# Optimization experiments

Measured on AMD Instinct MI355X. Metric: run time of the kernel, lower is better.

Reference implementation:

```python
import jax, jax.numpy as jnp
import numpy as np

B_DIM, C_DIM, K_DIM, L_DIM = 16, 64, 207, 64
SUPPORT_LEN, ORDER = 2, 2
C_IN = (ORDER * SUPPORT_LEN + 1) * C_DIM  # 320, include_self=True


def setup_inputs() -> dict:
    key = jax.random.key(0)
    k1, k2, k3, k4 = jax.random.split(key, 4)
    x = jax.random.normal(k1, (B_DIM, C_DIM, K_DIM * L_DIM), dtype=jnp.float32)
    # per-batch adaptive adjacencies (B, K, K), nonnegative like softmax(relu(E1 E2^T))
    a0 = jax.random.uniform(k2, (B_DIM, K_DIM, K_DIM), dtype=jnp.float32)
    a1 = jax.random.uniform(k3, (B_DIM, K_DIM, K_DIM), dtype=jnp.float32)
    # 1x1 conv weight (C_out, C_in) and bias
    W = jax.random.normal(k4, (C_DIM, C_IN), dtype=jnp.float32) * (1.0 / np.sqrt(C_IN))
    b = jnp.zeros((C_DIM,), dtype=jnp.float32)
    return {"x": x, "a0": a0, "a1": a1, "W": W, "b": b, "K": K_DIM, "L": L_DIM}


def reference(x, a0, a1, W, b, K, L):
    B, C = x.shape[0], x.shape[1]
    x = x.reshape(B, C, K, L)  # (B, C, K, L)
    # torch: x1[bl, c, j] = sum_k x[bl, c, k] * a[b, j, k]  (bmm with a^T)
    diffuse = lambda h, a: jnp.einsum('bckl,bjk->bcjl', h, a)
    out = [x]  # include_self=True
    for a in (a0, a1):
        x1 = diffuse(x, a)
        out.append(x1)
        for _ in range(2, ORDER + 1):
            x1 = diffuse(x1, a)
            out.append(x1)
    h = jnp.concatenate(out, axis=1)  # (B, 5C, K, L)
    y = jnp.einsum('bikl,oi->bokl', h, W) + b[None, :, None, None]  # 1x1 conv
    return y.reshape(B, C, K * L)
```

## Files before the change

### kernel.cpp

```cpp
#include <hip/hip_runtime.h>

typedef unsigned short u16;
typedef __bf16 bf16x8 __attribute__((ext_vector_type(8)));
typedef float f32x4 __attribute__((ext_vector_type(4)));

#define NB 16
#define NC 64
#define NK 207
#define NL 64
#define KP 224
#define NKL 13248
#define CIN 320


__device__ __forceinline__ u16 f2bf(float f) {
  unsigned u = __builtin_bit_cast(unsigned, f);
  u += 0x7FFFu + ((u >> 16) & 1u);
  return (u16)(u >> 16);
}

__device__ __forceinline__ void g2l16(const u16* gsrc, u16* ldst) {
  __builtin_amdgcn_global_load_lds(
      (const __attribute__((address_space(1))) unsigned int*)gsrc,
      (__attribute__((address_space(3))) unsigned int*)ldst, 16, 0, 0);
}

__global__ __launch_bounds__(256) void k_prep(
    const float* __restrict__ x, const float* __restrict__ a0,
    const float* __restrict__ a1, const float* __restrict__ W,
    u16* __restrict__ Xf, u16* __restrict__ Gf, u16* __restrict__ Wbf) {
  __shared__ __align__(16) u16 sm[32768];
  int id = blockIdx.x, t = threadIdx.x;
  if (id < 448) {
    int ks = id % 7;
    int rest = id / 7;
    int c4b = rest & 3, b = rest >> 2;
    int cl = t & 15, kp = t >> 4;
    int c = c4b * 16 + cl;
    int k0 = ks * 32 + kp * 2;
    const float* xrow = x + (size_t)(b * 64 + c) * NKL + (size_t)k0 * 64;
    bool in0 = (k0 < NK), in1 = (k0 + 1 < NK);
    unsigned* sm32 = (unsigned*)sm;
    int fi = (cl + 16 * (kp >> 2)) * 4 + (kp & 3);
#pragma unroll
    for (int g = 0; g < 4; g++) {
      float4 v0[4], v1[4];
#pragma unroll
      for (int i = 0; i < 4; i++) {
        float4 z = {0.f, 0.f, 0.f, 0.f};
        v0[i] = in0 ? *(const float4*)(xrow + g * 16 + i * 4) : z;
        v1[i] = in1 ? *(const float4*)(xrow + 64 + g * 16 + i * 4) : z;
      }
      const float* f0 = (const float*)v0;
      const float* f1 = (const float*)v1;
#pragma unroll
      for (int e2 = 0; e2 < 16; e2++) {
        int ll = g * 16 + e2;
        sm32[ll * 256 + fi] =
            (unsigned)f2bf(f0[e2]) | ((unsigned)f2bf(f1[e2]) << 16);
      }
    }
    __syncthreads();
    int wavei = t >> 6, lane = t & 63;
    u16* Xb = Xf + (size_t)b * 256 * 7 * 512;
    for (int f = wavei * 16; f < wavei * 16 + 16; f++) {
      bf16x8 v = *(const bf16x8*)&sm[f * 512 + lane * 8];
      *(bf16x8*)(Xb + ((size_t)(f * 4 + c4b) * 7 + ks) * 512 + lane * 8) = v;
    }
  } else if (id < 960) {
    int local = id - 448;
    int bw = local >> 4, tp = local & 15;
    int b = bw >> 1, w = bw & 1;
    int m0 = (tp >> 2) * 64, n0 = (tp & 3) * 64;
    const float* A = (w ? a1 : a0) + (size_t)b * NK * NK;
    for (int u = t; u < 64 * 28; u += 256) {
      int ml = u / 28, kc = u - ml * 28;
      int m = m0 + ml;
      u16 v[8] __attribute__((aligned(16)));
#pragma unroll
      for (int j = 0; j < 8; j++) {
        int k = kc * 8 + j;
        v[j] = (m < NK && k < NK) ? f2bf(A[(size_t)m * NK + k]) : (u16)0;
      }
      *(int4*)&sm[((ml >> 4) * 7 + (kc >> 2)) * 512 +
                  ((ml & 15) + 16 * (kc & 3)) * 8] = *(int4*)v;
    }
    {
      int nl = t & 63, mq = t >> 6;
      int n = n0 + nl;
      bool nin = (n < NK);
      unsigned* cm32 = (unsigned*)&sm[14336];
      for (int mi = 0; mi < 28; mi++) {
        int m = mq * 56 + mi * 2;
        u16 lo = (nin && m < NK) ? f2bf(A[(size_t)m * NK + n]) : (u16)0;
        u16 hi = (nin && m + 1 < NK) ? f2bf(A[(size_t)(m + 1) * NK + n]) : (u16)0;
        cm32[((nl >> 4) * 7 + (m >> 5)) * 256 +
             ((nl & 15) + 16 * ((m >> 3) & 3)) * 4 + ((m >> 1) & 3)] =
            (unsigned)lo | ((unsigned)hi << 16);
      }
    }
    __syncthreads();
    int lane = t & 63, wave = t >> 6;
    int r = lane & 15, q = lane >> 4;
    u16* Gp24 = Gf + ((size_t)b * 5 + 2 + 2 * w) * 13 * 7 * 512;
    for (int o = wave; o < 16; o += 4) {
      int mf = o >> 2, nf = o & 3;
      f32x4 acc = {};
#pragma unroll
      for (int ks = 0; ks < 7; ks++) {
        bf16x8 af = *(const bf16x8*)&sm[(mf * 7 + ks) * 512 + lane * 8];
        bf16x8 bg = *(const bf16x8*)&sm[14336 + (nf * 7 + ks) * 512 + lane * 8];
        acc = __builtin_amdgcn_mfma_f32_16x16x32_bf16(af, bg, acc, 0, 0, 0);
      }
#pragma unroll
      for (int rr = 0; rr < 4; rr++) {
        int mj = m0 + mf * 16 + q * 4 + rr;
        int nk = n0 + nf * 16 + r;
        if (mj < 208 && nk < KP)
          Gp24[((size_t)(mj >> 4) * 7 + (nk >> 5)) * 512 +
               ((mj & 15) + 16 * ((nk >> 3) & 3)) * 8 + (nk & 7)] =
              f2bf(acc[rr]);
      }
    }
  } else if (id < 1216) {
    int local = id - 960;
    int rt = local & 7, bw = local >> 3;
    int b = bw >> 1, w = bw & 1;
    const float* A = (w ? a1 : a0) + (size_t)b * NK * NK;
    u16* Gp13 = Gf + ((size_t)b * 5 + 1 + 2 * w) * 13 * 7 * 512;
    int m0 = rt * 26;
    for (int u = t; u < 26 * 28; u += 256) {
      int ml = u / 28, kc = u - ml * 28;
      int m = m0 + ml;
      u16 v[8] __attribute__((aligned(16)));
#pragma unroll
      for (int j = 0; j < 8; j++) {
        int k = kc * 8 + j;
        v[j] = (m < NK && k < NK) ? f2bf(A[(size_t)m * NK + k]) : (u16)0;
      }
      *(int4*)(Gp13 + ((size_t)(m >> 4) * 7 + (kc >> 2)) * 512 +
               ((m & 15) + 16 * (kc & 3)) * 8) = *(int4*)v;
    }
  } else if (id < 1248) {
    int local = id - 1216, b = local >> 1, half = local & 1;
    u16* Gp0 = Gf + (size_t)b * 5 * 13 * 7 * 512;
    for (int ci = t; ci < 104 * 28; ci += 256) {
      int jr = ci / 28, kc = ci - jr * 28;
      int j = half * 104 + jr;
      u16 v[8] __attribute__((aligned(16)));
      for (int jj = 0; jj < 8; jj++)
        v[jj] = (j == kc * 8 + jj && j < NK) ? (u16)0x3F80 : (u16)0;
      *(int4*)(Gp0 + ((size_t)(j >> 4) * 7 + (kc >> 2)) * 512 +
               ((j & 15) + 16 * (kc & 3)) * 8) = *(int4*)v;
    }
  } else {
    for (int ci = t; ci < 2560; ci += 256) {
      int o = ci / 40, kc = ci - o * 40;
      u16 v[8] __attribute__((aligned(16)));
      for (int j = 0; j < 8; j++) v[j] = f2bf(W[o * CIN + kc * 8 + j]);
      *(int4*)(Wbf + ((size_t)(o >> 4) * 10 + (kc >> 2)) * 512 +
               ((o & 15) + 16 * (kc & 3)) * 8) = *(int4*)v;
    }
  }
}

#define AG 17920
__global__ __launch_bounds__(512, 4) void k_fused(
    const u16* __restrict__ Gf, const u16* __restrict__ Xf,
    const u16* __restrict__ Wbf, const float* __restrict__ bias,
    float* __restrict__ y) {
  __shared__ __align__(16) u16 lds[AG + 2 * 8192];
  int id = blockIdx.x;
  int wg = (id & 7) * 416 + (id >> 3);
  int b = wg / 208, rem = wg % 208;
  int jt = rem >> 4, lt = rem & 15;
  int tid = threadIdx.x, wave = tid >> 6, lane = tid & 63;
  int r = lane & 15, q = lane >> 4;
  const u16* Gb = Gf + (size_t)b * 5 * 13 * 7 * 512;
  const u16* Xw = Xf + ((size_t)b * 256 + lt * 16) * 7 * 512;

  for (int i2 = 0; i2 < 5; i2++) {
    int tile = i2 * 8 + wave;
    if (tile < 35) {
      int p = tile / 7, ks = tile - p * 7;
      g2l16(Gb + ((size_t)(p * 13 + jt) * 7 + ks) * 512 + lane * 8,
            &lds[tile * 512 + lane * 8]);
    }
  }
  for (int i2 = 0; i2 < 2; i2++) {
    int tl = wave * 2 + i2;
    g2l16(Xw + (size_t)tl * 7 * 512 + lane * 8, &lds[AG + tl * 512 + lane * 8]);
  }
  asm volatile("s_waitcnt vmcnt(2)" ::: "memory");
  __builtin_amdgcn_s_barrier();

  f32x4 acc1[5][2] = {};
#pragma unroll
  for (int ks = 0; ks < 7; ks++) {
    int cur = ks & 1;
    if (ks < 6) {
      for (int i2 = 0; i2 < 2; i2++) {
        int tl = wave * 2 + i2;
        g2l16(Xw + ((size_t)tl * 7 + ks + 1) * 512 + lane * 8,
              &lds[AG + (cur ^ 1) * 8192 + tl * 512 + lane * 8]);
      }
      asm volatile("s_waitcnt vmcnt(2)" ::: "memory");
    } else {
      asm volatile("s_waitcnt vmcnt(0)" ::: "memory");
    }
    bf16x8 af0 = *(const bf16x8*)&lds[AG + cur * 8192 + (wave * 2 + 0) * 512 + lane * 8];
    bf16x8 af1 = *(const bf16x8*)&lds[AG + cur * 8192 + (wave * 2 + 1) * 512 + lane * 8];
    __builtin_amdgcn_s_setprio(1);
#pragma unroll
    for (int p = 0; p < 5; p++) {
      bf16x8 bg = *(const bf16x8*)&lds[(p * 7 + ks) * 512 + lane * 8];
      acc1[p][0] = __builtin_amdgcn_mfma_f32_16x16x32_bf16(af0, bg, acc1[p][0], 0, 0, 0);
      acc1[p][1] = __builtin_amdgcn_mfma_f32_16x16x32_bf16(af1, bg, acc1[p][1], 0, 0, 0);
    }
    __builtin_amdgcn_s_setprio(0);
  }
  __syncthreads();

#pragma unroll
  for (int p = 0; p < 5; p++)
#pragma unroll
    for (int mf = 0; mf < 2; mf++) {
      int m = (wave * 2 + mf) * 16 + q * 4;
      int tt = m >> 6, c = m & 63;
      int cs = c ^ ((r & 7) << 3);
      int idxT = ((p * 16 + r) * 4 + tt) * 72 + cs;
      u16 v0 = f2bf(acc1[p][mf][0]), v1 = f2bf(acc1[p][mf][1]);
      u16 v2 = f2bf(acc1[p][mf][2]), v3 = f2bf(acc1[p][mf][3]);
      *(uint2*)&lds[idxT] = make_uint2((unsigned)v0 | ((unsigned)v1 << 16),
                                       (unsigned)v2 | ((unsigned)v3 << 16));
    }
  int mo = wave >> 1, nh = (wave & 1) * 2;
  const u16* Wt = Wbf + (size_t)mo * 10 * 512 + lane * 8;
  bf16x8 aw[10];
#pragma unroll
  for (int ks = 0; ks < 10; ks++) aw[ks] = *(const bf16x8*)(Wt + ks * 512);
  __syncthreads();

  f32x4 acc2[2] = {};
#pragma unroll
  for (int ks = 0; ks < 10; ks++) {
    int p = ks >> 1, c0 = (ks & 1) * 32;
#pragma unroll
    for (int nf = 0; nf < 2; nf++) {
      int n = (nh + nf) * 16 + r;
      int j = n >> 2, tt = n & 3;
      int cs = (c0 + q * 8) ^ ((j & 7) << 3);
      bf16x8 bt = *(const bf16x8*)&lds[((p * 16 + j) * 4 + tt) * 72 + cs];
      acc2[nf] = __builtin_amdgcn_mfma_f32_16x16x32_bf16(aw[ks], bt, acc2[nf], 0, 0, 0);
    }
  }

  int o0 = mo * 16 + q * 4;
  float4 bv = *(const float4*)&bias[o0];
  float* yb = y + (size_t)b * 64 * NKL;
#pragma unroll
  for (int nf = 0; nf < 2; nf++) {
    int n = (nh + nf) * 16 + r;
    int j = n >> 2, tt = n & 3;
    int jnode = jt * 16 + j;
    if (jnode < NK) {
      int col = jnode * 64 + lt * 4 + tt;
      yb[(size_t)(o0 + 0) * NKL + col] = acc2[nf][0] + bv.x;
      yb[(size_t)(o0 + 1) * NKL + col] = acc2[nf][1] + bv.y;
      yb[(size_t)(o0 + 2) * NKL + col] = acc2[nf][2] + bv.z;
      yb[(size_t)(o0 + 3) * NKL + col] = acc2[nf][3] + bv.w;
    }
  }
}

extern "C" void kernel_launch(void* const* d_in, const int* in_sizes, int n_in,
                              void* d_out, int out_size, void* d_ws, size_t ws_size,
                              hipStream_t stream) {
  const float* x = (const float*)d_in[0];
  const float* a0 = (const float*)d_in[1];
  const float* a1 = (const float*)d_in[2];
  const float* W = (const float*)d_in[3];
  const float* bias = (const float*)d_in[4];
  float* y = (float*)d_out;
  char* ws = (char*)d_ws;

  size_t off = 0;
  auto alloc = [&](size_t bytes) {
    size_t o = off;
    off = (off + bytes + 511) & ~(size_t)511;
    return o;
  };
  size_t o_Xf = alloc((size_t)NB * 256 * 7 * 512 * 2);
  size_t o_Gf = alloc((size_t)NB * 5 * 13 * 7 * 512 * 2);
  size_t o_Wf = alloc((size_t)4 * 10 * 512 * 2);
  (void)ws_size;

  u16* Xf = (u16*)(ws + o_Xf);
  u16* Gf = (u16*)(ws + o_Gf);
  u16* Wf = (u16*)(ws + o_Wf);

  k_prep<<<dim3(1249), 256, 0, stream>>>(x, a0, a1, W, Xf, Gf, Wf);
  k_fused<<<dim3(16 * 13 * 16), 512, 0, stream>>>(Gf, Xf, Wf, bias, y);
}
```

Measured before the change: 235.9 us.

## Split prep kernel into finer blocks with smaller shared memory footprint

```diff
diff --git a/kernel.cpp b/kernel.cpp
--- a/kernel.cpp
+++ b/kernel.cpp
@@ -29,51 +29,52 @@
     const float* __restrict__ x, const float* __restrict__ a0,
     const float* __restrict__ a1, const float* __restrict__ W,
     u16* __restrict__ Xf, u16* __restrict__ Gf, u16* __restrict__ Wbf) {
-  __shared__ __align__(16) u16 sm[32768];
+  __shared__ __align__(16) u16 sm[14336];
   int id = blockIdx.x, t = threadIdx.x;
-  if (id < 448) {
+  if (id < 1792) {
     int ks = id % 7;
     int rest = id / 7;
-    int c4b = rest & 3, b = rest >> 2;
-    int cl = t & 15, kp = t >> 4;
-    int c = c4b * 16 + cl;
-    int k0 = ks * 32 + kp * 2;
-    const float* xrow = x + (size_t)(b * 64 + c) * NKL + (size_t)k0 * 64;
-    bool in0 = (k0 < NK), in1 = (k0 + 1 < NK);
-    unsigned* sm32 = (unsigned*)sm;
-    int fi = (cl + 16 * (kp >> 2)) * 4 + (kp & 3);
-#pragma unroll
-    for (int g = 0; g < 4; g++) {
-      float4 v0[4], v1[4];
-#pragma unroll
-      for (int i = 0; i < 4; i++) {
-        float4 z = {0.f, 0.f, 0.f, 0.f};
-        v0[i] = in0 ? *(const float4*)(xrow + g * 16 + i * 4) : z;
-        v1[i] = in1 ? *(const float4*)(xrow + 64 + g * 16 + i * 4) : z;
-      }
-      const float* f0 = (const float*)v0;
-      const float* f1 = (const float*)v1;
-#pragma unroll
-      for (int e2 = 0; e2 < 16; e2++) {
-        int ll = g * 16 + e2;
-        sm32[ll * 256 + fi] =
-            (unsigned)f2bf(f0[e2]) | ((unsigned)f2bf(f1[e2]) << 16);
-      }
+    int lh = rest & 3, c4 = (rest >> 2) & 3, b = rest >> 4;
+    int l0 = lh * 16;
+    int cl = t & 15, kl = t >> 4;
+    const float* xc = x + (size_t)(b * 64 + c4 * 16 + cl) * NKL;
+#pragma unroll
+    for (int kki = 0; kki < 2; kki++) {
+      int kk = kl + kki * 16;
+      int k = ks * 32 + kk;
+      float4 v0 = {0.f, 0.f, 0.f, 0.f}, v1 = v0, v2 = v0, v3 = v0;
+      if (k < NK) {
+        const float4* p = (const float4*)(xc + (size_t)k * 64 + l0);
+        v0 = p[0]; v1 = p[1]; v2 = p[2]; v3 = p[3];
+      }
+      int q = kk >> 3, e = kk & 7;
+      u16* dst = &sm[(cl + 16 * q) * 8 + e];
+      dst[0 * 512] = f2bf(v0.x);   dst[1 * 512] = f2bf(v0.y);
+      dst[2 * 512] = f2bf(v0.z);   dst[3 * 512] = f2bf(v0.w);
+      dst[4 * 512] = f2bf(v1.x);   dst[5 * 512] = f2bf(v1.y);
+      dst[6 * 512] = f2bf(v1.z);   dst[7 * 512] = f2bf(v1.w);
+      dst[8 * 512] = f2bf(v2.x);   dst[9 * 512] = f2bf(v2.y);
+      dst[10 * 512] = f2bf(v2.z);  dst[11 * 512] = f2bf(v2.w);
+      dst[12 * 512] = f2bf(v3.x);  dst[13 * 512] = f2bf(v3.y);
+      dst[14 * 512] = f2bf(v3.z);  dst[15 * 512] = f2bf(v3.w);
     }
     __syncthreads();
     int wavei = t >> 6, lane = t & 63;
     u16* Xb = Xf + (size_t)b * 256 * 7 * 512;
-    for (int f = wavei * 16; f < wavei * 16 + 16; f++) {
+#pragma unroll
+    for (int i = 0; i < 4; i++) {
+      int f = wavei * 4 + i;
       bf16x8 v = *(const bf16x8*)&sm[f * 512 + lane * 8];
-      *(bf16x8*)(Xb + ((size_t)(f * 4 + c4b) * 7 + ks) * 512 + lane * 8) = v;
-    }
-  } else if (id < 960) {
-    int local = id - 448;
-    int bw = local >> 4, tp = local & 15;
+      *(bf16x8*)(Xb + ((size_t)((l0 + f) * 4 + c4) * 7 + ks) * 512 +
+                 lane * 8) = v;
+    }
+  } else if (id < 3360) {
+    int local = id - 1792;
+    int bw = local / 49, tl = local % 49;
     int b = bw >> 1, w = bw & 1;
-    int m0 = (tp >> 2) * 64, n0 = (tp & 3) * 64;
+    int m0 = (tl / 7) * 32, n0 = (tl % 7) * 32;
     const float* A = (w ? a1 : a0) + (size_t)b * NK * NK;
-    for (int u = t; u < 64 * 28; u += 256) {
+    for (int u = t; u < 32 * 28; u += 256) {
       int ml = u / 28, kc = u - ml * 28;
       int m = m0 + ml;
       u16 v[8] __attribute__((aligned(16)));
@@ -86,12 +87,12 @@
                   ((ml & 15) + 16 * (kc & 3)) * 8] = *(int4*)v;
     }
     {
-      int nl = t & 63, mq = t >> 6;
+      int nl = t & 31, mq = t >> 5;
       int n = n0 + nl;
       bool nin = (n < NK);
-      unsigned* cm32 = (unsigned*)&sm[14336];
-      for (int mi = 0; mi < 28; mi++) {
-        int m = mq * 56 + mi * 2;
+      unsigned* cm32 = (unsigned*)&sm[7168];
+      for (int mi = 0; mi < 14; mi++) {
+        int m = mq * 28 + mi * 2;
         u16 lo = (nin && m < NK) ? f2bf(A[(size_t)m * NK + n]) : (u16)0;
         u16 hi = (nin && m + 1 < NK) ? f2bf(A[(size_t)(m + 1) * NK + n]) : (u16)0;
         cm32[((nl >> 4) * 7 + (m >> 5)) * 256 +
@@ -103,27 +104,27 @@
     int lane = t & 63, wave = t >> 6;
     int r = lane & 15, q = lane >> 4;
     u16* Gp24 = Gf + ((size_t)b * 5 + 2 + 2 * w) * 13 * 7 * 512;
-    for (int o = wave; o < 16; o += 4) {
-      int mf = o >> 2, nf = o & 3;
+    {
+      int mf = wave >> 1, nf = wave & 1;
       f32x4 acc = {};
 #pragma unroll
       for (int ks = 0; ks < 7; ks++) {
         bf16x8 af = *(const bf16x8*)&sm[(mf * 7 + ks) * 512 + lane * 8];
-        bf16x8 bg = *(const bf16x8*)&sm[14336 + (nf * 7 + ks) * 512 + lane * 8];
+        bf16x8 bg = *(const bf16x8*)&sm[7168 + (nf * 7 + ks) * 512 + lane * 8];
         acc = __builtin_amdgcn_mfma_f32_16x16x32_bf16(af, bg, acc, 0, 0, 0);
       }
 #pragma unroll
       for (int rr = 0; rr < 4; rr++) {
         int mj = m0 + mf * 16 + q * 4 + rr;
         int nk = n0 + nf * 16 + r;
-        if (mj < 208 && nk < KP)
+        if (mj < 208)
           Gp24[((size_t)(mj >> 4) * 7 + (nk >> 5)) * 512 +
                ((mj & 15) + 16 * ((nk >> 3) & 3)) * 8 + (nk & 7)] =
               f2bf(acc[rr]);
       }
     }
-  } else if (id < 1216) {
-    int local = id - 960;
+  } else if (id < 3616) {
+    int local = id - 3360;
     int rt = local & 7, bw = local >> 3;
     int b = bw >> 1, w = bw & 1;
     const float* A = (w ? a1 : a0) + (size_t)b * NK * NK;
@@ -141,8 +142,8 @@
       *(int4*)(Gp13 + ((size_t)(m >> 4) * 7 + (kc >> 2)) * 512 +
                ((m & 15) + 16 * (kc & 3)) * 8) = *(int4*)v;
     }
-  } else if (id < 1248) {
-    int local = id - 1216, b = local >> 1, half = local & 1;
+  } else if (id < 3648) {
+    int local = id - 3616, b = local >> 1, half = local & 1;
     u16* Gp0 = Gf + (size_t)b * 5 * 13 * 7 * 512;
     for (int ci = t; ci < 104 * 28; ci += 256) {
       int jr = ci / 28, kc = ci - jr * 28;
@@ -299,6 +300,6 @@
   u16* Gf = (u16*)(ws + o_Gf);
   u16* Wf = (u16*)(ws + o_Wf);
 
-  k_prep<<<dim3(1249), 256, 0, stream>>>(x, a0, a1, W, Xf, Gf, Wf);
+  k_prep<<<dim3(3649), 256, 0, stream>>>(x, a0, a1, W, Xf, Gf, Wf);
   k_fused<<<dim3(16 * 13 * 16), 512, 0, stream>>>(Gf, Xf, Wf, bias, y);
 }
```

New measurement: 209.6 us. 11.1% less time.
